# Kernel tuning notes

Hardware: AMD Instinct MI355X
Metric: run time of the kernel (lower is better)

The kernel has to match this reference:

```python
import jax, jax.numpy as jnp
import numpy as np

G = 131072      # number of agent groups (batched graphs)
N_AGENTS = 6    # 5 search parties + 1 helicopter, fully-connected graph per group
D_IN = 64       # input_dim
H = 64          # hidden_dim (conv1 out)
GH = 64         # gnn_hidden (conv2 out, MLP hidden)
OUT = 2         # actor action dim
N_TYPES = 2     # agent types: search party (0), helicopter (1)


def setup_inputs() -> dict:
    key = jax.random.key(0)
    ks = jax.random.split(key, 20)
    s = 0.05
    inp = {
        'obs': jax.random.normal(ks[0], (G, N_AGENTS, D_IN), jnp.float32),
        # SAGEConv('pool') layer 1: fc_pool (in->in), fc_self, fc_neigh, bias
        'Wp1': jax.random.normal(ks[1], (D_IN, D_IN), jnp.float32) * s,
        'bp1': jnp.zeros((D_IN,), jnp.float32),
        'Ws1': jax.random.normal(ks[2], (D_IN, H), jnp.float32) * s,
        'Wn1': jax.random.normal(ks[3], (D_IN, H), jnp.float32) * s,
        'b1': jnp.zeros((H,), jnp.float32),
        # SAGEConv('pool') layer 2
        'Wp2': jax.random.normal(ks[4], (H, H), jnp.float32) * s,
        'bp2': jnp.zeros((H,), jnp.float32),
        'Ws2': jax.random.normal(ks[5], (H, GH), jnp.float32) * s,
        'Wn2': jax.random.normal(ks[6], (H, GH), jnp.float32) * s,
        'b2': jnp.zeros((GH,), jnp.float32),
        # per-agent-type actor MLPs (stacked over type axis t=2)
        'MW1': jax.random.normal(ks[7], (N_TYPES, GH, GH), jnp.float32) * s,
        'Mb1': jnp.zeros((N_TYPES, GH), jnp.float32),
        'MW2': jax.random.normal(ks[8], (N_TYPES, GH, GH), jnp.float32) * s,
        'Mb2': jnp.zeros((N_TYPES, GH), jnp.float32),
        'MW3': jax.random.normal(ks[9], (N_TYPES, GH, GH), jnp.float32) * s,
        'Mb3': jnp.zeros((N_TYPES, GH), jnp.float32),
        'MW4': jax.random.uniform(ks[10], (N_TYPES, GH, OUT), jnp.float32, -0.003, 0.003),
        'Mb4': jnp.zeros((N_TYPES, OUT), jnp.float32),
    }
    return inp


def _sage_pool(x, Wp, bp, Ws, Wn, b):
    # DGL SAGEConv aggregator_type='pool' on a fully-connected graph w/ self loops:
    # neigh_j = max_i relu(fc_pool(x_i)); rst = fc_self(x) + fc_neigh(neigh) + bias
    p = jax.nn.relu(x @ Wp + bp)              # [G, n, din]
    neigh = p.max(axis=1, keepdims=True)      # [G, 1, din] (all nodes are neighbors)
    return x @ Ws + neigh @ Wn + b            # [G, n, dout]


def reference(obs, Wp1, bp1, Ws1, Wn1, b1, Wp2, bp2, Ws2, Wn2, b2,
              MW1, Mb1, MW2, Mb2, MW3, Mb3, MW4, Mb4):
    h = jnp.tanh(_sage_pool(obs, Wp1, bp1, Ws1, Wn1, b1))   # conv1 + Tanh activation
    h = _sage_pool(h, Wp2, bp2, Ws2, Wn2, b2)               # conv2 (no activation)
    res = h.mean(axis=1)                                     # AvgPooling per graph -> [G, GH]
    # per-agent-type MLPs, batched over type axis t
    x = jax.nn.relu(jnp.einsum('gd,tdh->tgh', res, MW1) + Mb1[:, None, :])
    x = jax.nn.relu(jnp.einsum('tgh,thk->tgk', x, MW2) + Mb2[:, None, :])
    x = jax.nn.relu(jnp.einsum('tgh,thk->tgk', x, MW3) + Mb3[:, None, :])
    out_t = jnp.tanh(jnp.einsum('tgh,tho->tgo', x, MW4) + Mb4[:, None, :])  # [T, G, 2]
    agent_types = jnp.array([0, 0, 0, 0, 0, 1])  # 5 search parties + 1 helicopter
    return jnp.transpose(out_t[agent_types], (1, 0, 2))     # [G, 6, 2]
```

## Files before the change

kernel.cpp:

```cpp
#include <hip/hip_runtime.h>
#include <math.h>


typedef _Float16 f16;
typedef __fp16   fp16x2_t __attribute__((ext_vector_type(2)));
typedef _Float16 half4_t  __attribute__((ext_vector_type(4)));
typedef _Float16 half8_t  __attribute__((ext_vector_type(8)));
typedef float    float4_t __attribute__((ext_vector_type(4)));

#define NW 8
#define LDS_PAD_F 17920

#define MFMA16(A,B,C) __builtin_amdgcn_mfma_f32_16x16x16f16((A),(B),(C),0,0,0)

__device__ __forceinline__ float fast_tanh(float x) {
    float e = __expf(2.0f * x);
    return 1.0f - 2.0f / (e + 1.0f);
}

__device__ __forceinline__ float4_t max4(float4_t a, float4_t b) {
    float4_t r;
    r[0] = fmaxf(a[0], b[0]); r[1] = fmaxf(a[1], b[1]);
    r[2] = fmaxf(a[2], b[2]); r[3] = fmaxf(a[3], b[3]);
    return r;
}

__device__ __forceinline__ float4_t bcast4(float v) {
    float4_t r; r[0] = v; r[1] = v; r[2] = v; r[3] = v; return r;
}

__device__ __forceinline__ half4_t flo(half8_t v) {
    half4_t r; r[0] = v[0]; r[1] = v[1]; r[2] = v[2]; r[3] = v[3]; return r;
}
__device__ __forceinline__ half4_t fhi(half8_t v) {
    half4_t r; r[0] = v[4]; r[1] = v[5]; r[2] = v[6]; r[3] = v[7]; return r;
}

__device__ __forceinline__ half4_t cvt4(float4_t v) {
    fp16x2_t p0 = __builtin_amdgcn_cvt_pkrtz(v[0], v[1]);
    fp16x2_t p1 = __builtin_amdgcn_cvt_pkrtz(v[2], v[3]);
    half4_t r;
    r[0] = (f16)p0[0]; r[1] = (f16)p0[1]; r[2] = (f16)p1[0]; r[3] = (f16)p1[1];
    return r;
}

__global__ void prep_weights(const float* __restrict__ Wp1, const float* __restrict__ Ws1,
                             const float* __restrict__ Wn1, const float* __restrict__ Wp2,
                             const float* __restrict__ Ws2, const float* __restrict__ Wn2,
                             const float* __restrict__ MW1, const float* __restrict__ MW2,
                             const float* __restrict__ MW3, const float* __restrict__ MW4,
                             f16* __restrict__ img)
{
    const int m = blockIdx.x;
    const int tid = threadIdx.x;
    if (m < 12) {
        const float* src;
        switch (m) {
            case 0: src = Wp1; break;  case 1: src = Ws1; break;
            case 2: src = Wn1; break;  case 3: src = Wp2; break;
            case 4: src = Ws2; break;  case 5: src = Wn2; break;
            case 6: src = MW1; break;  case 7: src = MW2; break;
            case 8: src = MW3; break;  case 9: src = MW1 + 4096; break;
            case 10: src = MW2 + 4096; break; default: src = MW3 + 4096; break;
        }
        for (int e = tid; e < 4096; e += 256) {
            const int p = e >> 9, mt = p >> 1, kp = p & 1;
            const int o = e & 511, lane = o >> 3, j8 = o & 7;
            const int kt = kp * 2 + (j8 >> 2), j = j8 & 3;
            const int k = kt * 16 + (lane >> 4) * 4 + j;
            const int n = mt * 16 + (lane & 15);
            img[m * 4096 + e] = (f16)src[k * 64 + n];
        }
    } else {
        for (int e = tid; e < 2048; e += 256) {
            const int ty = e >> 10, o = e & 1023;
            const int kp = o >> 9, oo = o & 511, lane = oo >> 3, j8 = oo & 7;
            const int kt = kp * 2 + (j8 >> 2), j = j8 & 3;
            const int k = kt * 16 + (lane >> 4) * 4 + j;
            const int mm = lane & 15;
            float v = 0.f;
            if (ty == 0) { if (mm < 10) v = MW4[k * 2 + (mm & 1)]; }
            else         { if (mm == 10 || mm == 11) v = MW4[128 + k * 2 + (mm & 1)]; }
            img[12 * 4096 + e] = (f16)v;
        }
    }
}

__global__ __launch_bounds__(512, 2)
void gnn_mfma(const float* __restrict__ obs, const f16* __restrict__ img,
              const float* __restrict__ bp1, const float* __restrict__ b1,
              const float* __restrict__ bp2, const float* __restrict__ b2,
              const float* __restrict__ Mb1, const float* __restrict__ Mb2,
              const float* __restrict__ Mb3, const float* __restrict__ Mb4,
              float* __restrict__ out)
{
    __shared__ __align__(16) float smem[LDS_PAD_F];
    const int tid  = threadIdx.x;
    if (tid == 0) { volatile float* g = smem; g[0] = 0.f; }

    const int w    = __builtin_amdgcn_readfirstlane(tid >> 6);
    const int l    = tid & 63;
    const int col  = l & 15;
    const int quad = l >> 4;

    const int wid = blockIdx.x * NW + w;
    const int g0  = wid * 16;
    const float* orow = obs + (size_t)(g0 + col) * 384 + quad * 4;

    half8_t W[4][2];
    auto loadWmat = [&](int baseH) {
        #pragma unroll
        for (int mt = 0; mt < 4; ++mt)
            #pragma unroll
            for (int kp = 0; kp < 2; ++kp)
                W[mt][kp] = *(const half8_t*)(img + baseH + (mt * 2 + kp) * 512 + l * 8);
    };
    auto wfrag = [&](int mt, int kt) -> half4_t {
        return (kt & 1) ? fhi(W[mt][kt >> 1]) : flo(W[mt][kt >> 1]);
    };

    loadWmat(0);
    float4_t bq[4];
    #pragma unroll
    for (int mt = 0; mt < 4; ++mt)
        bq[mt] = *(const float4_t*)(bp1 + mt * 16 + quad * 4);

    float4_t n1[4];
    #pragma unroll
    for (int mt = 0; mt < 4; ++mt) n1[mt] = bcast4(0.f);
    {
        float4_t ox[4];
        #pragma unroll
        for (int kt = 0; kt < 4; ++kt)
            ox[kt] = *(const float4_t*)(orow + kt * 16);
        #pragma unroll
        for (int a = 0; a < 6; ++a) {
            half4_t ob[4];
            #pragma unroll
            for (int kt = 0; kt < 4; ++kt) ob[kt] = cvt4(ox[kt]);
            if (a < 5) {
                #pragma unroll
                for (int kt = 0; kt < 4; ++kt)
                    ox[kt] = *(const float4_t*)(orow + (a + 1) * 64 + kt * 16);
            }
            #pragma unroll
            for (int mt = 0; mt < 4; ++mt) {
                float4_t acc = bq[mt];
                #pragma unroll
                for (int kt = 0; kt < 4; ++kt)
                    acc = MFMA16(wfrag(mt, kt), ob[kt], acc);
                n1[mt] = max4(n1[mt], acc);
            }
        }
    }

    half4_t n1h[4];
    #pragma unroll
    for (int kt = 0; kt < 4; ++kt) n1h[kt] = cvt4(n1[kt]);
    float4_t c[4];
    {
        int bW = 2 * 4096;
        asm volatile("" : "+s"(bW));
        loadWmat(bW);
        #pragma unroll
        for (int mt = 0; mt < 4; ++mt) {
            float4_t acc = *(const float4_t*)(b1 + mt * 16 + quad * 4);
            #pragma unroll
            for (int kt = 0; kt < 4; ++kt)
                acc = MFMA16(wfrag(mt, kt), n1h[kt], acc);
            c[mt] = acc;
        }
    }

    size_t orp = (size_t)orow;
    asm volatile("" : "+v"(orp));
    const float* orow2 = (const float*)orp;
    {
        int bWs = 1 * 4096;
        asm volatile("" : "+s"(bWs));
        loadWmat(bWs);
    }
    half4_t hh[6][4];
    float4_t hbar[4];
    #pragma unroll
    for (int mt = 0; mt < 4; ++mt) hbar[mt] = bcast4(0.f);
    #pragma unroll
    for (int a = 0; a < 6; ++a) {
        half4_t ob[4];
        #pragma unroll
        for (int kt = 0; kt < 4; ++kt)
            ob[kt] = cvt4(*(const float4_t*)(orow2 + a * 64 + kt * 16));
        #pragma unroll
        for (int mt = 0; mt < 4; ++mt) {
            float4_t acc = c[mt];
            #pragma unroll
            for (int kt = 0; kt < 4; ++kt)
                acc = MFMA16(wfrag(mt, kt), ob[kt], acc);
            #pragma unroll
            for (int r = 0; r < 4; ++r) acc[r] = fast_tanh(acc[r]);
            hbar[mt] += acc;
            hh[a][mt] = cvt4(acc);
        }
    }

    float4_t n2[4];
    {
        int bWp = 3 * 4096;
        asm volatile("" : "+s"(bWp));
        loadWmat(bWp);
        float4_t bp2q[4];
        #pragma unroll
        for (int mt = 0; mt < 4; ++mt)
            bp2q[mt] = *(const float4_t*)(bp2 + mt * 16 + quad * 4);
        #pragma unroll
        for (int mt = 0; mt < 4; ++mt) n2[mt] = bcast4(0.f);
        #pragma unroll
        for (int a = 0; a < 6; ++a) {
            #pragma unroll
            for (int mt = 0; mt < 4; ++mt) {
                float4_t q = bp2q[mt];
                #pragma unroll
                for (int kt = 0; kt < 4; ++kt)
                    q = MFMA16(wfrag(mt, kt), hh[a][kt], q);
                n2[mt] = max4(n2[mt], q);
            }
        }
    }

    half4_t hbh[4], n2h[4];
    #pragma unroll
    for (int kt = 0; kt < 4; ++kt) {
        hbh[kt] = cvt4(hbar[kt] * (1.0f / 6.0f));
        n2h[kt] = cvt4(n2[kt]);
    }
    float4_t rr[4];
    {
        int b4 = 4 * 4096;
        asm volatile("" : "+s"(b4));
        loadWmat(b4);
        #pragma unroll
        for (int mt = 0; mt < 4; ++mt) {
            float4_t acc = *(const float4_t*)(b2 + mt * 16 + quad * 4);
            #pragma unroll
            for (int kt = 0; kt < 4; ++kt)
                acc = MFMA16(wfrag(mt, kt), hbh[kt], acc);
            rr[mt] = acc;
        }
    }
    {
        int b5 = 5 * 4096;
        asm volatile("" : "+s"(b5));
        loadWmat(b5);
        #pragma unroll
        for (int mt = 0; mt < 4; ++mt) {
            #pragma unroll
            for (int kt = 0; kt < 4; ++kt)
                rr[mt] = MFMA16(wfrag(mt, kt), n2h[kt], rr[mt]);
        }
    }

    half4_t x3h[2][4];
    #pragma unroll
    for (int ty = 0; ty < 2; ++ty) {
        half4_t xh[4];
        #pragma unroll
        for (int kt = 0; kt < 4; ++kt) xh[kt] = cvt4(rr[kt]);
        #pragma unroll
        for (int layer = 0; layer < 3; ++layer) {
            int bb = (6 + ty * 3 + layer) * 4096;
            asm volatile("" : "+s"(bb));
            loadWmat(bb);
            const float* Mb = (layer == 0 ? Mb1 : layer == 1 ? Mb2 : Mb3) + ty * 64;
            float4_t nx[4];
            #pragma unroll
            for (int mt = 0; mt < 4; ++mt) {
                float4_t acc = *(const float4_t*)(Mb + mt * 16 + quad * 4);
                #pragma unroll
                for (int kt = 0; kt < 4; ++kt)
                    acc = MFMA16(wfrag(mt, kt), xh[kt], acc);
                nx[mt] = max4(acc, bcast4(0.f));
            }
            #pragma unroll
            for (int kt = 0; kt < 4; ++kt) xh[kt] = cvt4(nx[kt]);
        }
        #pragma unroll
        for (int kt = 0; kt < 4; ++kt) x3h[ty][kt] = xh[kt];
    }

    float4_t d = bcast4(0.f);
    {
        int bh = 12 * 4096;
        asm volatile("" : "+s"(bh));
        half8_t H0[2], H1[2];
        #pragma unroll
        for (int kp = 0; kp < 2; ++kp) {
            H0[kp] = *(const half8_t*)(img + bh + kp * 512 + l * 8);
            H1[kp] = *(const half8_t*)(img + bh + 1024 + kp * 512 + l * 8);
        }
        #pragma unroll
        for (int kt = 0; kt < 4; ++kt) {
            half4_t f = (kt & 1) ? fhi(H0[kt >> 1]) : flo(H0[kt >> 1]);
            d = MFMA16(f, x3h[0][kt], d);
        }
        #pragma unroll
        for (int kt = 0; kt < 4; ++kt) {
            half4_t f = (kt & 1) ? fhi(H1[kt >> 1]) : flo(H1[kt >> 1]);
            d = MFMA16(f, x3h[1][kt], d);
        }
    }

    if (quad < 3) {
        const float m00 = Mb4[0], m01 = Mb4[1], m10 = Mb4[2], m11 = Mb4[3];
        float4_t v;
        #pragma unroll
        for (int r = 0; r < 4; ++r) {
            const int slot = quad * 4 + r;
            const float mb = (slot < 10) ? ((r & 1) ? m01 : m00)
                                         : ((r & 1) ? m11 : m10);
            v[r] = fast_tanh(d[r] + mb);
        }
        *(float4_t*)(out + (size_t)(g0 + col) * 12 + quad * 4) = v;
    }
}

extern "C" void kernel_launch(void* const* d_in, const int* in_sizes, int n_in,
                              void* d_out, int out_size, void* d_ws, size_t ws_size,
                              hipStream_t stream)
{
    const float* obs = (const float*)d_in[0];
    const float* Wp1 = (const float*)d_in[1];
    const float* bp1 = (const float*)d_in[2];
    const float* Ws1 = (const float*)d_in[3];
    const float* Wn1 = (const float*)d_in[4];
    const float* b1  = (const float*)d_in[5];
    const float* Wp2 = (const float*)d_in[6];
    const float* bp2 = (const float*)d_in[7];
    const float* Ws2 = (const float*)d_in[8];
    const float* Wn2 = (const float*)d_in[9];
    const float* b2  = (const float*)d_in[10];
    const float* MW1 = (const float*)d_in[11];
    const float* Mb1 = (const float*)d_in[12];
    const float* MW2 = (const float*)d_in[13];
    const float* Mb2 = (const float*)d_in[14];
    const float* MW3 = (const float*)d_in[15];
    const float* Mb3 = (const float*)d_in[16];
    const float* MW4 = (const float*)d_in[17];
    const float* Mb4 = (const float*)d_in[18];
    float* out = (float*)d_out;
    f16* img = (f16*)d_ws;

    hipLaunchKernelGGL(prep_weights, dim3(13), dim3(256), 0, stream,
                       Wp1, Ws1, Wn1, Wp2, Ws2, Wn2, MW1, MW2, MW3, MW4, img);
    hipLaunchKernelGGL(gnn_mfma, dim3(1024), dim3(512), 0, stream,
                       obs, img, bp1, b1, bp2, b2, Mb1, Mb2, Mb3, Mb4, out);
}
```

Measured before the change: 394.5 us.

## Process two 16-group tiles per wavefront and fuse conv2 pool into conv1 loop

Each wavefront now handles 32 groups as two 16-column tiles, so every weight fragment loaded from global memory feeds two MFMA chains. This halves weight reloads per group and exposes more independent MFMAs. The Wp2 pool matmul and its max now run inside the conv1 self-term loop with a second weight register set, so the six per-agent hidden tiles no longer need to stay live. The bias and ReLU for the pool are applied after the max, which is equivalent because both are monotone. Block size drops to 256 threads with a 3-blocks occupancy hint and a smaller LDS pad, at the cost of higher register pressure.

```diff
diff --git a/kernel.cpp b/kernel.cpp
--- a/kernel.cpp
+++ b/kernel.cpp
@@ -8,8 +8,8 @@
 typedef _Float16 half8_t  __attribute__((ext_vector_type(8)));
 typedef float    float4_t __attribute__((ext_vector_type(4)));
 
-#define NW 8
-#define LDS_PAD_F 17920
+#define NW 4
+#define LDS_PAD_F 13568
 
 #define MFMA16(A,B,C) __builtin_amdgcn_mfma_f32_16x16x16f16((A),(B),(C),0,0,0)
 
@@ -86,7 +86,7 @@
     }
 }
 
-__global__ __launch_bounds__(512, 2)
+__global__ __launch_bounds__(256, 3)
 void gnn_mfma(const float* __restrict__ obs, const f16* __restrict__ img,
               const float* __restrict__ bp1, const float* __restrict__ b1,
               const float* __restrict__ bp2, const float* __restrict__ b2,
@@ -104,190 +104,230 @@
     const int quad = l >> 4;
 
     const int wid = blockIdx.x * NW + w;
-    const int g0  = wid * 16;
-    const float* orow = obs + (size_t)(g0 + col) * 384 + quad * 4;
-
-    half8_t W[4][2];
-    auto loadWmat = [&](int baseH) {
+    const int g0  = wid * 32;
+    const float* orow[2];
+    orow[0] = obs + (size_t)(g0 + col) * 384 + quad * 4;
+    orow[1] = obs + (size_t)(g0 + 16 + col) * 384 + quad * 4;
+
+    half8_t Wm[4][2], Wn[4][2];
+    auto loadW = [&](half8_t (&Wd)[4][2], int baseH) {
         #pragma unroll
         for (int mt = 0; mt < 4; ++mt)
             #pragma unroll
             for (int kp = 0; kp < 2; ++kp)
-                W[mt][kp] = *(const half8_t*)(img + baseH + (mt * 2 + kp) * 512 + l * 8);
+                Wd[mt][kp] = *(const half8_t*)(img + baseH + (mt * 2 + kp) * 512 + l * 8);
     };
-    auto wfrag = [&](int mt, int kt) -> half4_t {
-        return (kt & 1) ? fhi(W[mt][kt >> 1]) : flo(W[mt][kt >> 1]);
+    auto wf = [&](const half8_t (&Wd)[4][2], int mt, int kt) -> half4_t {
+        return (kt & 1) ? fhi(Wd[mt][kt >> 1]) : flo(Wd[mt][kt >> 1]);
     };
 
-    loadWmat(0);
+    loadW(Wm, 0);
     float4_t bq[4];
     #pragma unroll
     for (int mt = 0; mt < 4; ++mt)
         bq[mt] = *(const float4_t*)(bp1 + mt * 16 + quad * 4);
 
-    float4_t n1[4];
-    #pragma unroll
-    for (int mt = 0; mt < 4; ++mt) n1[mt] = bcast4(0.f);
-    {
-        float4_t ox[4];
-        #pragma unroll
-        for (int kt = 0; kt < 4; ++kt)
-            ox[kt] = *(const float4_t*)(orow + kt * 16);
+    float4_t n1[2][4];
+    #pragma unroll
+    for (int b = 0; b < 2; ++b)
+        #pragma unroll
+        for (int mt = 0; mt < 4; ++mt) n1[b][mt] = bcast4(0.f);
+    {
+        float4_t ox[2][4];
+        #pragma unroll
+        for (int b = 0; b < 2; ++b)
+            #pragma unroll
+            for (int kt = 0; kt < 4; ++kt)
+                ox[b][kt] = *(const float4_t*)(orow[b] + kt * 16);
         #pragma unroll
         for (int a = 0; a < 6; ++a) {
-            half4_t ob[4];
-            #pragma unroll
-            for (int kt = 0; kt < 4; ++kt) ob[kt] = cvt4(ox[kt]);
+            half4_t ob[2][4];
+            #pragma unroll
+            for (int b = 0; b < 2; ++b)
+                #pragma unroll
+                for (int kt = 0; kt < 4; ++kt) ob[b][kt] = cvt4(ox[b][kt]);
             if (a < 5) {
                 #pragma unroll
-                for (int kt = 0; kt < 4; ++kt)
-                    ox[kt] = *(const float4_t*)(orow + (a + 1) * 64 + kt * 16);
+                for (int b = 0; b < 2; ++b)
+                    #pragma unroll
+                    for (int kt = 0; kt < 4; ++kt)
+                        ox[b][kt] = *(const float4_t*)(orow[b] + (a + 1) * 64 + kt * 16);
             }
             #pragma unroll
             for (int mt = 0; mt < 4; ++mt) {
-                float4_t acc = bq[mt];
-                #pragma unroll
-                for (int kt = 0; kt < 4; ++kt)
-                    acc = MFMA16(wfrag(mt, kt), ob[kt], acc);
-                n1[mt] = max4(n1[mt], acc);
-            }
-        }
-    }
-
-    half4_t n1h[4];
-    #pragma unroll
-    for (int kt = 0; kt < 4; ++kt) n1h[kt] = cvt4(n1[kt]);
-    float4_t c[4];
+                #pragma unroll
+                for (int b = 0; b < 2; ++b) {
+                    float4_t acc = bq[mt];
+                    #pragma unroll
+                    for (int kt = 0; kt < 4; ++kt)
+                        acc = MFMA16(wf(Wm, mt, kt), ob[b][kt], acc);
+                    n1[b][mt] = max4(n1[b][mt], acc);
+                }
+            }
+        }
+    }
+
+    half4_t n1h[2][4];
+    #pragma unroll
+    for (int b = 0; b < 2; ++b)
+        #pragma unroll
+        for (int kt = 0; kt < 4; ++kt) n1h[b][kt] = cvt4(n1[b][kt]);
+    float4_t c[2][4];
     {
         int bW = 2 * 4096;
         asm volatile("" : "+s"(bW));
-        loadWmat(bW);
+        loadW(Wm, bW);
         #pragma unroll
         for (int mt = 0; mt < 4; ++mt) {
-            float4_t acc = *(const float4_t*)(b1 + mt * 16 + quad * 4);
+            const float4_t bb = *(const float4_t*)(b1 + mt * 16 + quad * 4);
+            #pragma unroll
+            for (int b = 0; b < 2; ++b) {
+                float4_t acc = bb;
+                #pragma unroll
+                for (int kt = 0; kt < 4; ++kt)
+                    acc = MFMA16(wf(Wm, mt, kt), n1h[b][kt], acc);
+                c[b][mt] = acc;
+            }
+        }
+    }
+
+    {
+        int bWs = 1 * 4096, bWp = 3 * 4096;
+        asm volatile("" : "+s"(bWs), "+s"(bWp));
+        loadW(Wm, bWs);
+        loadW(Wn, bWp);
+    }
+    float4_t hbar[2][4], n2m[2][4];
+    #pragma unroll
+    for (int b = 0; b < 2; ++b)
+        #pragma unroll
+        for (int mt = 0; mt < 4; ++mt) {
+            hbar[b][mt] = bcast4(0.f);
+            n2m[b][mt]  = bcast4(-3.0e38f);
+        }
+    #pragma unroll
+    for (int a = 0; a < 6; ++a) {
+        half4_t ob[2][4];
+        #pragma unroll
+        for (int b = 0; b < 2; ++b)
             #pragma unroll
             for (int kt = 0; kt < 4; ++kt)
-                acc = MFMA16(wfrag(mt, kt), n1h[kt], acc);
-            c[mt] = acc;
-        }
-    }
-
-    size_t orp = (size_t)orow;
-    asm volatile("" : "+v"(orp));
-    const float* orow2 = (const float*)orp;
-    {
-        int bWs = 1 * 4096;
-        asm volatile("" : "+s"(bWs));
-        loadWmat(bWs);
-    }
-    half4_t hh[6][4];
-    float4_t hbar[4];
-    #pragma unroll
-    for (int mt = 0; mt < 4; ++mt) hbar[mt] = bcast4(0.f);
-    #pragma unroll
-    for (int a = 0; a < 6; ++a) {
-        half4_t ob[4];
-        #pragma unroll
-        for (int kt = 0; kt < 4; ++kt)
-            ob[kt] = cvt4(*(const float4_t*)(orow2 + a * 64 + kt * 16));
+                ob[b][kt] = cvt4(*(const float4_t*)(orow[b] + a * 64 + kt * 16));
+        half4_t hh[2][4];
         #pragma unroll
         for (int mt = 0; mt < 4; ++mt) {
-            float4_t acc = c[mt];
-            #pragma unroll
-            for (int kt = 0; kt < 4; ++kt)
-                acc = MFMA16(wfrag(mt, kt), ob[kt], acc);
-            #pragma unroll
-            for (int r = 0; r < 4; ++r) acc[r] = fast_tanh(acc[r]);
-            hbar[mt] += acc;
-            hh[a][mt] = cvt4(acc);
-        }
-    }
-
-    float4_t n2[4];
-    {
-        int bWp = 3 * 4096;
-        asm volatile("" : "+s"(bWp));
-        loadWmat(bWp);
-        float4_t bp2q[4];
-        #pragma unroll
-        for (int mt = 0; mt < 4; ++mt)
-            bp2q[mt] = *(const float4_t*)(bp2 + mt * 16 + quad * 4);
-        #pragma unroll
-        for (int mt = 0; mt < 4; ++mt) n2[mt] = bcast4(0.f);
-        #pragma unroll
-        for (int a = 0; a < 6; ++a) {
-            #pragma unroll
-            for (int mt = 0; mt < 4; ++mt) {
-                float4_t q = bp2q[mt];
+            #pragma unroll
+            for (int b = 0; b < 2; ++b) {
+                float4_t acc = c[b][mt];
                 #pragma unroll
                 for (int kt = 0; kt < 4; ++kt)
-                    q = MFMA16(wfrag(mt, kt), hh[a][kt], q);
-                n2[mt] = max4(n2[mt], q);
-            }
-        }
-    }
-
-    half4_t hbh[4], n2h[4];
-    #pragma unroll
-    for (int kt = 0; kt < 4; ++kt) {
-        hbh[kt] = cvt4(hbar[kt] * (1.0f / 6.0f));
-        n2h[kt] = cvt4(n2[kt]);
-    }
-    float4_t rr[4];
+                    acc = MFMA16(wf(Wm, mt, kt), ob[b][kt], acc);
+                #pragma unroll
+                for (int r = 0; r < 4; ++r) acc[r] = fast_tanh(acc[r]);
+                hbar[b][mt] += acc;
+                hh[b][mt] = cvt4(acc);
+            }
+        }
+        #pragma unroll
+        for (int mt = 0; mt < 4; ++mt) {
+            #pragma unroll
+            for (int b = 0; b < 2; ++b) {
+                float4_t q = bcast4(0.f);
+                #pragma unroll
+                for (int kt = 0; kt < 4; ++kt)
+                    q = MFMA16(wf(Wn, mt, kt), hh[b][kt], q);
+                n2m[b][mt] = max4(n2m[b][mt], q);
+            }
+        }
+    }
+    float4_t n2[2][4];
+    #pragma unroll
+    for (int mt = 0; mt < 4; ++mt) {
+        const float4_t bb = *(const float4_t*)(bp2 + mt * 16 + quad * 4);
+        #pragma unroll
+        for (int b = 0; b < 2; ++b)
+            n2[b][mt] = max4(n2m[b][mt] + bb, bcast4(0.f));
+    }
+
+    half4_t hbh[2][4], n2h[2][4];
+    #pragma unroll
+    for (int b = 0; b < 2; ++b)
+        #pragma unroll
+        for (int kt = 0; kt < 4; ++kt) {
+            hbh[b][kt] = cvt4(hbar[b][kt] * (1.0f / 6.0f));
+            n2h[b][kt] = cvt4(n2[b][kt]);
+        }
+    float4_t rr[2][4];
     {
         int b4 = 4 * 4096;
         asm volatile("" : "+s"(b4));
-        loadWmat(b4);
+        loadW(Wm, b4);
         #pragma unroll
         for (int mt = 0; mt < 4; ++mt) {
-            float4_t acc = *(const float4_t*)(b2 + mt * 16 + quad * 4);
-            #pragma unroll
-            for (int kt = 0; kt < 4; ++kt)
-                acc = MFMA16(wfrag(mt, kt), hbh[kt], acc);
-            rr[mt] = acc;
+            const float4_t bb = *(const float4_t*)(b2 + mt * 16 + quad * 4);
+            #pragma unroll
+            for (int b = 0; b < 2; ++b) {
+                float4_t acc = bb;
+                #pragma unroll
+                for (int kt = 0; kt < 4; ++kt)
+                    acc = MFMA16(wf(Wm, mt, kt), hbh[b][kt], acc);
+                rr[b][mt] = acc;
+            }
         }
     }
     {
         int b5 = 5 * 4096;
         asm volatile("" : "+s"(b5));
-        loadWmat(b5);
-        #pragma unroll
-        for (int mt = 0; mt < 4; ++mt) {
-            #pragma unroll
-            for (int kt = 0; kt < 4; ++kt)
-                rr[mt] = MFMA16(wfrag(mt, kt), n2h[kt], rr[mt]);
-        }
-    }
-
-    half4_t x3h[2][4];
+        loadW(Wm, b5);
+        #pragma unroll
+        for (int mt = 0; mt < 4; ++mt)
+            #pragma unroll
+            for (int b = 0; b < 2; ++b)
+                #pragma unroll
+                for (int kt = 0; kt < 4; ++kt)
+                    rr[b][mt] = MFMA16(wf(Wm, mt, kt), n2h[b][kt], rr[b][mt]);
+    }
+
+    half4_t x3h[2][2][4];
     #pragma unroll
     for (int ty = 0; ty < 2; ++ty) {
-        half4_t xh[4];
-        #pragma unroll
-        for (int kt = 0; kt < 4; ++kt) xh[kt] = cvt4(rr[kt]);
+        half4_t xh[2][4];
+        #pragma unroll
+        for (int b = 0; b < 2; ++b)
+            #pragma unroll
+            for (int kt = 0; kt < 4; ++kt) xh[b][kt] = cvt4(rr[b][kt]);
         #pragma unroll
         for (int layer = 0; layer < 3; ++layer) {
             int bb = (6 + ty * 3 + layer) * 4096;
             asm volatile("" : "+s"(bb));
-            loadWmat(bb);
+            loadW(Wm, bb);
             const float* Mb = (layer == 0 ? Mb1 : layer == 1 ? Mb2 : Mb3) + ty * 64;
-            float4_t nx[4];
+            float4_t nx[2][4];
             #pragma unroll
             for (int mt = 0; mt < 4; ++mt) {
-                float4_t acc = *(const float4_t*)(Mb + mt * 16 + quad * 4);
-                #pragma unroll
-                for (int kt = 0; kt < 4; ++kt)
-                    acc = MFMA16(wfrag(mt, kt), xh[kt], acc);
-                nx[mt] = max4(acc, bcast4(0.f));
-            }
-            #pragma unroll
-            for (int kt = 0; kt < 4; ++kt) xh[kt] = cvt4(nx[kt]);
-        }
-        #pragma unroll
-        for (int kt = 0; kt < 4; ++kt) x3h[ty][kt] = xh[kt];
-    }
-
-    float4_t d = bcast4(0.f);
+                const float4_t bv = *(const float4_t*)(Mb + mt * 16 + quad * 4);
+                #pragma unroll
+                for (int b = 0; b < 2; ++b) {
+                    float4_t acc = bv;
+                    #pragma unroll
+                    for (int kt = 0; kt < 4; ++kt)
+                        acc = MFMA16(wf(Wm, mt, kt), xh[b][kt], acc);
+                    nx[b][mt] = max4(acc, bcast4(0.f));
+                }
+            }
+            #pragma unroll
+            for (int b = 0; b < 2; ++b)
+                #pragma unroll
+                for (int kt = 0; kt < 4; ++kt) xh[b][kt] = cvt4(nx[b][kt]);
+        }
+        #pragma unroll
+        for (int b = 0; b < 2; ++b)
+            #pragma unroll
+            for (int kt = 0; kt < 4; ++kt) x3h[ty][b][kt] = xh[b][kt];
+    }
+
+    float4_t d[2];
+    d[0] = bcast4(0.f); d[1] = bcast4(0.f);
     {
         int bh = 12 * 4096;
         asm volatile("" : "+s"(bh));
@@ -299,27 +339,32 @@
         }
         #pragma unroll
         for (int kt = 0; kt < 4; ++kt) {
-            half4_t f = (kt & 1) ? fhi(H0[kt >> 1]) : flo(H0[kt >> 1]);
-            d = MFMA16(f, x3h[0][kt], d);
+            const half4_t f = (kt & 1) ? fhi(H0[kt >> 1]) : flo(H0[kt >> 1]);
+            #pragma unroll
+            for (int b = 0; b < 2; ++b) d[b] = MFMA16(f, x3h[0][b][kt], d[b]);
         }
         #pragma unroll
         for (int kt = 0; kt < 4; ++kt) {
-            half4_t f = (kt & 1) ? fhi(H1[kt >> 1]) : flo(H1[kt >> 1]);
-            d = MFMA16(f, x3h[1][kt], d);
+            const half4_t f = (kt & 1) ? fhi(H1[kt >> 1]) : flo(H1[kt >> 1]);
+            #pragma unroll
+            for (int b = 0; b < 2; ++b) d[b] = MFMA16(f, x3h[1][b][kt], d[b]);
         }
     }
 
     if (quad < 3) {
         const float m00 = Mb4[0], m01 = Mb4[1], m10 = Mb4[2], m11 = Mb4[3];
-        float4_t v;
-        #pragma unroll
-        for (int r = 0; r < 4; ++r) {
-            const int slot = quad * 4 + r;
-            const float mb = (slot < 10) ? ((r & 1) ? m01 : m00)
-                                         : ((r & 1) ? m11 : m10);
-            v[r] = fast_tanh(d[r] + mb);
-        }
-        *(float4_t*)(out + (size_t)(g0 + col) * 12 + quad * 4) = v;
+        #pragma unroll
+        for (int b = 0; b < 2; ++b) {
+            float4_t v;
+            #pragma unroll
+            for (int r = 0; r < 4; ++r) {
+                const int slot = quad * 4 + r;
+                const float mb = (slot < 10) ? ((r & 1) ? m01 : m00)
+                                             : ((r & 1) ? m11 : m10);
+                v[r] = fast_tanh(d[b][r] + mb);
+            }
+            *(float4_t*)(out + (size_t)(g0 + b * 16 + col) * 12 + quad * 4) = v;
+        }
     }
 }
 
@@ -351,6 +396,6 @@
 
     hipLaunchKernelGGL(prep_weights, dim3(13), dim3(256), 0, stream,
                        Wp1, Ws1, Wn1, Wp2, Ws2, Wn2, MW1, MW2, MW3, MW4, img);
-    hipLaunchKernelGGL(gnn_mfma, dim3(1024), dim3(512), 0, stream,
+    hipLaunchKernelGGL(gnn_mfma, dim3(1024), dim3(256), 0, stream,
                        obs, img, bp1, b1, bp2, b2, Mb1, Mb2, Mb3, Mb4, out);
 }
```

Result: slower. 467.1 us (+18.4%).
